# Optimization experiments

Hardware: AMD Instinct MI355X
Metric: run time of the kernel (lower is better)

The kernel has to match this reference:

```python
import jax, jax.numpy as jnp
import numpy as np

B, S, D = 2, 2048, 2048
KVH, QPG, HD = 8, 4, 64          # kv heads, q heads per group, head size
THETA = 1024.0
PARTIAL = 0.5
SOFT_CAP = 50.0
EPS = 1e-5


def setup_inputs() -> dict:
    key = jax.random.key(0)
    ks = jax.random.split(key, 8)
    scale = 0.02
    return {
        "x": jax.random.normal(ks[0], (B, S, D), jnp.float32),
        "wq": jax.random.normal(ks[1], (KVH, QPG, HD, D), jnp.float32) * scale,
        "wk": jax.random.normal(ks[2], (KVH, HD, D), jnp.float32) * scale,
        "wv": jax.random.normal(ks[3], (KVH, HD, D), jnp.float32) * scale,
        "wo": jax.random.normal(ks[4], (D, KVH, QPG, HD), jnp.float32) * scale,
        "qn_w": jnp.ones((HD,), jnp.float32),
        "kn_w": jnp.ones((HD,), jnp.float32),
        "pos_ids": jnp.arange(S, dtype=jnp.int32),
    }


def _rms_norm(t, w):
    var = jnp.mean(jnp.square(t), axis=-1, keepdims=True)
    return t * jax.lax.rsqrt(var + EPS) * w


def _rope_tables(pos_ids):
    half = HD // 2
    rotated_size = int(HD * PARTIAL)
    inv_freq = 1.0 / THETA ** (jnp.arange(0, 2 * half, 2, dtype=jnp.float32) / rotated_size)
    inv_freq = jnp.where(jnp.arange(half) < rotated_size // 2, inv_freq, 0.0)
    freqs = pos_ids.astype(jnp.float32)[:, None] * inv_freq[None, :]   # [S, half]
    emb = jnp.concatenate([freqs, freqs], axis=-1)                      # [S, HD]
    return jnp.cos(emb), jnp.sin(emb)


def _apply_rope(t, cos, sin):
    # t: [..., S, HD]; rotate_half: (x1, x2) -> (-x2, x1)
    half = HD // 2
    x1, x2 = t[..., :half], t[..., half:]
    rot = jnp.concatenate([-x2, x1], axis=-1)
    return t * cos + rot * sin


def reference(x, wq, wk, wv, wo, qn_w, kn_w, pos_ids):
    # QKV projections (GQA)
    q = jnp.einsum("bsd,gphd->bgpsh", x, wq)   # [B,KVH,QPG,S,HD]
    k = jnp.einsum("bsd,ghd->bgsh", x, wk)      # [B,KVH,S,HD]
    v = jnp.einsum("bsd,ghd->bgsh", x, wv)

    # QK-norm (RMS over head dim)
    q = _rms_norm(q, qn_w)
    k = _rms_norm(k, kn_w)

    # partial RoPE
    cos, sin = _rope_tables(pos_ids)            # [S, HD]
    q = _apply_rope(q, cos, sin).astype(x.dtype)
    k = _apply_rope(k, cos, sin).astype(x.dtype)

    # attention in fp32 (upcast_attn) with soft cap and causal mask
    scale = 1.0 / jnp.sqrt(jnp.float32(HD))
    scores = jnp.einsum("bgpsh,bgth->bgpst", q.astype(jnp.float32), k.astype(jnp.float32)) * scale
    scores = SOFT_CAP * jnp.tanh(scores / SOFT_CAP)
    causal = pos_ids[:, None] >= pos_ids[None, :]                    # [S, S]
    scores = jnp.where(causal, scores, jnp.finfo(jnp.float32).min)
    probs = jax.nn.softmax(scores, axis=-1)
    attn = jnp.einsum("bgpst,bgth->bgpsh", probs, v.astype(jnp.float32)).astype(x.dtype)

    # output projection (flatten kv_head x q_heads_per_group -> heads)
    out = jnp.einsum("bgpsh,dgph->bsd", attn, wo)
    return out
```

## Files before the change

### kernel.cpp

```cpp
#include <hip/hip_runtime.h>
#include <stdint.h>

#define S_LEN   2048
#define D_MODEL 2048
#define N_KVH   8
#define N_QPG   4
#define N_HD    64

typedef __attribute__((ext_vector_type(8))) short  short8;
typedef __attribute__((ext_vector_type(4))) short  short4v;
typedef __attribute__((ext_vector_type(4))) float  float4v;

__device__ __forceinline__ unsigned short f2bf(float x) {
    unsigned int u = __float_as_uint(x);
    u = (u + 0x7fffu + ((u >> 16) & 1u)) >> 16;
    return (unsigned short)u;
}

__device__ __forceinline__ void gload_lds16(const unsigned short* g, unsigned short* l) {
    __builtin_amdgcn_global_load_lds((const __attribute__((address_space(1))) unsigned int*)g,
                                     (__attribute__((address_space(3))) unsigned int*)l,
                                     16, 0, 0);
}

__device__ __forceinline__ short8 lds_read8(const unsigned short* p) {
    union { short8 s8; short4v s4[2]; } u;
    u.s4[0] = *(const short4v*)p;
    u.s4[1] = *(const short4v*)(p + 4);
    return u.s8;
}

__global__ __launch_bounds__(256) void cvt_all(const float* __restrict__ x,
                                               const float* __restrict__ wq,
                                               const float* __restrict__ wk,
                                               const float* __restrict__ wv,
                                               const float* __restrict__ wo,
                                               unsigned short* __restrict__ xb,
                                               unsigned short* __restrict__ wqb,
                                               unsigned short* __restrict__ wkb,
                                               unsigned short* __restrict__ wvb,
                                               unsigned short* __restrict__ wob) {
    size_t i = (size_t)blockIdx.x * 256 + threadIdx.x;
    const float* src; unsigned short* dst; size_t off;
    if      (i < 1048576) { src = x;  dst = xb;  off = i; }
    else if (i < 1572864) { src = wq; dst = wqb; off = i - 1048576; }
    else if (i < 1703936) { src = wk; dst = wkb; off = i - 1572864; }
    else if (i < 1835008) { src = wv; dst = wvb; off = i - 1703936; }
    else                  { src = wo; dst = wob; off = i - 1835008; }
    const float4* p = (const float4*)src + off * 2;
    float4 a = p[0], b = p[1];
    union { unsigned short us[8]; uint4 v; } u;
    u.us[0] = f2bf(a.x); u.us[1] = f2bf(a.y); u.us[2] = f2bf(a.z); u.us[3] = f2bf(a.w);
    u.us[4] = f2bf(b.x); u.us[5] = f2bf(b.y); u.us[6] = f2bf(b.z); u.us[7] = f2bf(b.w);
    ((uint4*)dst)[off] = u.v;
}

#define GSTAGE(AL, BL, KO)                         \
    gload_lds16(Ag + (KO),          (AL));         \
    gload_lds16(Ag + 16 * K + (KO), (AL) + 512);   \
    gload_lds16(Bg + (KO),          (BL));         \
    gload_lds16(Bg + 16 * K + (KO), (BL) + 512);

#define GCOMPUTE(OFF)                                                          \
    {                                                                          \
        short8 af[4], bf[4];                                                   \
        _Pragma("unroll")                                                      \
        for (int mt = 0; mt < 4; mt++)                                         \
            af[mt] = *(const short8*)(Alds + (OFF) + (wm + mt * 16 + l15) * 32 + quad * 8); \
        _Pragma("unroll")                                                      \
        for (int nt = 0; nt < 4; nt++)                                         \
            bf[nt] = *(const short8*)(Blds + (OFF) + (wn + nt * 16 + l15) * 32 + quad * 8); \
        _Pragma("unroll")                                                      \
        for (int mt = 0; mt < 4; mt++)                                         \
            _Pragma("unroll")                                                  \
            for (int nt = 0; nt < 4; nt++)                                     \
                acc[mt][nt] = __builtin_amdgcn_mfma_f32_16x16x32_bf16(         \
                    af[mt], bf[nt], acc[mt][nt], 0, 0, 0);                     \
    }

__global__ __launch_bounds__(256)
void gemm_qkv(const unsigned short* __restrict__ xb,
              const unsigned short* __restrict__ wqb,
              const unsigned short* __restrict__ wkb,
              const unsigned short* __restrict__ wvb,
              unsigned short* __restrict__ qout,
              unsigned short* __restrict__ kout,
              unsigned short* __restrict__ vtout,
              const float* __restrict__ qnw,
              const float* __restrict__ knw)
{
    __shared__ __align__(16) unsigned short Alds[2 * 128 * 32];
    __shared__ __align__(16) unsigned short Blds[2 * 128 * 32];

    const int tid  = threadIdx.x;
    const int lane = tid & 63;
    const int wave = tid >> 6;
    const int quad = lane >> 4;
    const int l15  = lane & 15;
    const int bx = blockIdx.x, by = blockIdx.y;
    const int role = (by < 16) ? 0 : (by < 20 ? 1 : 2);
    const unsigned short* A;
    const unsigned short* B;
    int m0, n0;
    if (role == 0)      { A = xb;  B = wqb; m0 = bx * 128; n0 = by * 128; }
    else if (role == 1) { A = xb;  B = wkb; m0 = bx * 128; n0 = (by - 16) * 128; }
    else                { A = wvb; B = xb;  m0 = (by - 20) * 128; n0 = bx * 128; }
    const int K = 2048;
    const int wm = (wave >> 1) * 64;
    const int wn = (wave & 1) * 64;

    float4v acc[4][4];
#pragma unroll
    for (int i = 0; i < 4; i++)
#pragma unroll
        for (int j = 0; j < 4; j++) acc[i][j] = (float4v){0.f, 0.f, 0.f, 0.f};

    const int j0 = wave * 2;
    const int lr = lane >> 2;
    const int lc = (lane & 3) * 8;
    const unsigned short* Ag = A + (size_t)(m0 + j0 * 16 + lr) * K + lc;
    const unsigned short* Bg = B + (size_t)(n0 + j0 * 16 + lr) * K + lc;
    unsigned short* Al0 = Alds + j0 * 512;
    unsigned short* Bl0 = Blds + j0 * 512;
    unsigned short* Al1 = Alds + 4096 + j0 * 512;
    unsigned short* Bl1 = Blds + 4096 + j0 * 512;

    GSTAGE(Al0, Bl0, 0);
    __syncthreads();

    for (int k0 = 0; k0 < K; k0 += 64) {
        GSTAGE(Al1, Bl1, k0 + 32);
        GCOMPUTE(0);
        __syncthreads();
        if (k0 + 64 < K) { GSTAGE(Al0, Bl0, k0 + 64); }
        GCOMPUTE(4096);
        __syncthreads();
    }

    const int nb = n0 + wn;
    const float* nw = (role == 1) ? knw : qnw;
#pragma unroll
    for (int mt = 0; mt < 4; mt++) {
#pragma unroll
        for (int r = 0; r < 4; r++) {
            const int m = m0 + wm + mt * 16 + quad * 4 + r;
            if (role == 2) {
#pragma unroll
                for (int nt = 0; nt < 4; nt++) {
                    int n = nb + nt * 16 + l15;
                    vtout[((size_t)(n >> 11) * 512 + m) * 2048 + (n & 2047)] =
                        f2bf(acc[mt][nt][r]);
                }
            } else {
                float v0 = acc[mt][0][r], v1 = acc[mt][1][r], v2 = acc[mt][2][r], v3 = acc[mt][3][r];
                float s2 = v0 * v0 + v1 * v1 + v2 * v2 + v3 * v3;
#pragma unroll
                for (int off = 1; off < 16; off <<= 1) s2 += __shfl_xor(s2, off, 64);
                float rs = rsqrtf(s2 * (1.0f / 64.0f) + 1e-5f);
                float nv0 = v0 * rs * nw[0 * 16 + l15];
                float nv1 = v1 * rs * nw[1 * 16 + l15];
                float nv2 = v2 * rs * nw[2 * 16 + l15];
                float nv3 = v3 * rs * nw[3 * 16 + l15];
                const int bidx = m >> 11, s = m & 2047;
                float ang = (float)s * exp2f(-0.625f * (float)l15);
                float sn, cs;
                __sincosf(ang, &sn, &cs);
                float o0 = nv0 * cs - nv2 * sn;
                float o2 = nv2 * cs + nv0 * sn;
                unsigned short* dst;
                if (role == 0) {
                    const int g = nb >> 8, p = (nb >> 6) & 3;
                    dst = qout + ((((size_t)bidx * N_KVH + g) * N_QPG + p) * S_LEN + s) * N_HD;
                } else {
                    const int g = nb >> 6;
                    dst = kout + (((size_t)bidx * N_KVH + g) * S_LEN + s) * N_HD;
                }
                dst[0 * 16 + l15] = f2bf(o0);
                dst[1 * 16 + l15] = f2bf(nv1);
                dst[2 * 16 + l15] = f2bf(o2);
                dst[3 * 16 + l15] = f2bf(nv3);
            }
        }
    }
}

__global__ __launch_bounds__(256)
void gemm_out(const unsigned short* __restrict__ A,
              const unsigned short* __restrict__ B,
              float* __restrict__ C,
              int M, int N, int K)
{
    __shared__ __align__(16) unsigned short Alds[2 * 128 * 32];
    __shared__ __align__(16) unsigned short Blds[2 * 128 * 32];

    const int tid  = threadIdx.x;
    const int lane = tid & 63;
    const int wave = tid >> 6;
    const int quad = lane >> 4;
    const int l15  = lane & 15;
    const int m0 = blockIdx.x * 128;
    const int n0 = blockIdx.y * 128;
    const int wm = (wave >> 1) * 64;
    const int wn = (wave & 1) * 64;

    float4v acc[4][4];
#pragma unroll
    for (int i = 0; i < 4; i++)
#pragma unroll
        for (int j = 0; j < 4; j++) acc[i][j] = (float4v){0.f, 0.f, 0.f, 0.f};

    const int j0 = wave * 2;
    const int lr = lane >> 2;
    const int lc = (lane & 3) * 8;
    const unsigned short* Ag = A + (size_t)(m0 + j0 * 16 + lr) * K + lc;
    const unsigned short* Bg = B + (size_t)(n0 + j0 * 16 + lr) * K + lc;
    unsigned short* Al0 = Alds + j0 * 512;
    unsigned short* Bl0 = Blds + j0 * 512;
    unsigned short* Al1 = Alds + 4096 + j0 * 512;
    unsigned short* Bl1 = Blds + 4096 + j0 * 512;

    GSTAGE(Al0, Bl0, 0);
    __syncthreads();

    for (int k0 = 0; k0 < K; k0 += 64) {
        GSTAGE(Al1, Bl1, k0 + 32);
        GCOMPUTE(0);
        __syncthreads();
        if (k0 + 64 < K) { GSTAGE(Al0, Bl0, k0 + 64); }
        GCOMPUTE(4096);
        __syncthreads();
    }

    const int nb = n0 + wn;
#pragma unroll
    for (int mt = 0; mt < 4; mt++) {
#pragma unroll
        for (int r = 0; r < 4; r++) {
            const int m = m0 + wm + mt * 16 + quad * 4 + r;
#pragma unroll
            for (int nt = 0; nt < 4; nt++) {
                int n = nb + nt * 16 + l15;
                C[(size_t)m * N + n] = acc[mt][nt][r];
            }
        }
    }
}

#define PSTRIDE 68

__global__ __launch_bounds__(256)
void attn_kernel(const unsigned short* __restrict__ Q,
                 const unsigned short* __restrict__ Kb,
                 const unsigned short* __restrict__ Vt,
                 unsigned short* __restrict__ O)
{
    __shared__ __align__(16) unsigned short Plds[4 * 32 * PSTRIDE];

    const int tid  = threadIdx.x;
    const int lane = tid & 63;
    const int w    = tid >> 6;
    const int quad = lane >> 4;
    const int l15  = lane & 15;
    const int qx = blockIdx.y;
    const int bg = blockIdx.x;
    const int b = bg >> 3, g = bg & 7;

    const unsigned short* qbase  = Q  + (((size_t)b * N_KVH + g) * N_QPG + w) * S_LEN * N_HD;
    const unsigned short* kbase  = Kb + ((size_t)b * N_KVH + g) * S_LEN * N_HD;
    const unsigned short* vtbase = Vt + ((size_t)b * N_KVH + g) * (size_t)N_HD * S_LEN;

    unsigned short* Pw = Plds + w * (32 * PSTRIDE);

    for (int half = 0; half < 2; half++) {
        const int qt = half ? (63 - qx) : qx;
        const int qrow0 = qt * 32;

        short8 qf[2][2];
#pragma unroll
        for (int mt = 0; mt < 2; mt++)
#pragma unroll
            for (int ks = 0; ks < 2; ks++)
                qf[mt][ks] = *(const short8*)(qbase + (size_t)(qrow0 + mt * 16 + l15) * N_HD + ks * 32 + quad * 8);

        float4v o_acc[2][4];
#pragma unroll
        for (int mt = 0; mt < 2; mt++)
#pragma unroll
            for (int nt = 0; nt < 4; nt++) o_acc[mt][nt] = (float4v){0.f, 0.f, 0.f, 0.f};
        float rsum[2][4];
#pragma unroll
        for (int mt = 0; mt < 2; mt++)
#pragma unroll
            for (int r = 0; r < 4; r++) rsum[mt][r] = 0.f;

        const int ktend = qrow0 >> 6;

        short8 kf[4][2];
#pragma unroll
        for (int nt = 0; nt < 4; nt++)
#pragma unroll
            for (int ks = 0; ks < 2; ks++)
                kf[nt][ks] = *(const short8*)(kbase + (size_t)(nt * 16 + l15) * N_HD + ks * 32 + quad * 8);

        for (int kt = 0; kt <= ktend; kt++) {
            float4v s_acc[2][4];
#pragma unroll
            for (int mt = 0; mt < 2; mt++)
#pragma unroll
                for (int nt = 0; nt < 4; nt++) s_acc[mt][nt] = (float4v){0.f, 0.f, 0.f, 0.f};
            __builtin_amdgcn_s_setprio(1);
#pragma unroll
            for (int ks = 0; ks < 2; ks++)
#pragma unroll
                for (int mt = 0; mt < 2; mt++)
#pragma unroll
                    for (int nt = 0; nt < 4; nt++)
                        s_acc[mt][nt] = __builtin_amdgcn_mfma_f32_16x16x32_bf16(qf[mt][ks], kf[nt][ks], s_acc[mt][nt], 0, 0, 0);
            __builtin_amdgcn_s_setprio(0);

            short8 vf[4][2];
#pragma unroll
            for (int nt = 0; nt < 4; nt++)
#pragma unroll
                for (int ks = 0; ks < 2; ks++)
                    vf[nt][ks] = *(const short8*)(vtbase + (size_t)(nt * 16 + l15) * S_LEN + kt * 64 + ks * 32 + quad * 8);

            if (kt < ktend) {
#pragma unroll
                for (int nt = 0; nt < 4; nt++)
#pragma unroll
                    for (int ks = 0; ks < 2; ks++)
                        kf[nt][ks] = *(const short8*)(kbase + (size_t)((kt + 1) * 64 + nt * 16 + l15) * N_HD + ks * 32 + quad * 8);
            }

            const bool diag = (kt == ktend);
#pragma unroll
            for (int mt = 0; mt < 2; mt++) {
#pragma unroll
                for (int r = 0; r < 4; r++) {
                    const int s_q  = qrow0 + mt * 16 + quad * 4 + r;
                    const int prow = (mt * 16 + quad * 4 + r) * PSTRIDE;
#pragma unroll
                    for (int nt = 0; nt < 4; nt++) {
                        float a = s_acc[mt][nt][r];
                        float u = a * a;
                        float wv = fmaf(u, -3.757018e-7f, 0.18033688f);
                        float p = __builtin_amdgcn_exp2f(fmaf(a, wv, -72.13475204f));
                        if (diag) {
                            int s_k = kt * 64 + nt * 16 + l15;
                            p = (s_k <= s_q) ? p : 0.0f;
                        }
                        rsum[mt][r] += p;
                        Pw[prow + nt * 16 + l15] =
                            (unsigned short)((__float_as_uint(p) + 0x8000u) >> 16);
                    }
                }
            }

#pragma unroll
            for (int ks = 0; ks < 2; ks++) {
                short8 pf[2];
#pragma unroll
                for (int mt = 0; mt < 2; mt++)
                    pf[mt] = lds_read8(Pw + (mt * 16 + l15) * PSTRIDE + ks * 32 + quad * 8);
                __builtin_amdgcn_s_setprio(1);
#pragma unroll
                for (int mt = 0; mt < 2; mt++)
#pragma unroll
                    for (int nt = 0; nt < 4; nt++)
                        o_acc[mt][nt] = __builtin_amdgcn_mfma_f32_16x16x32_bf16(pf[mt], vf[nt][ks], o_acc[mt][nt], 0, 0, 0);
                __builtin_amdgcn_s_setprio(0);
            }
        }

#pragma unroll
        for (int mt = 0; mt < 2; mt++) {
#pragma unroll
            for (int r = 0; r < 4; r++) {
                float s = rsum[mt][r];
                s += __shfl_xor(s, 1, 64);
                s += __shfl_xor(s, 2, 64);
                s += __shfl_xor(s, 4, 64);
                s += __shfl_xor(s, 8, 64);
                float inv = 1.0f / s;
                int s_q = qrow0 + mt * 16 + quad * 4 + r;
                size_t rowoff = ((size_t)(b * S_LEN + s_q)) * D_MODEL + (g * N_QPG + w) * N_HD;
#pragma unroll
                for (int nt = 0; nt < 4; nt++)
                    O[rowoff + nt * 16 + l15] = f2bf(o_acc[mt][nt][r] * inv);
            }
        }
    }
}

extern "C" void kernel_launch(void* const* d_in, const int* in_sizes, int n_in,
                              void* d_out, int out_size, void* d_ws, size_t ws_size,
                              hipStream_t stream)
{
    const float* x    = (const float*)d_in[0];
    const float* wq   = (const float*)d_in[1];
    const float* wk   = (const float*)d_in[2];
    const float* wv   = (const float*)d_in[3];
    const float* wo   = (const float*)d_in[4];
    const float* qn_w = (const float*)d_in[5];
    const float* kn_w = (const float*)d_in[6];

    char* ws = (char*)d_ws;
    unsigned short* xb  = (unsigned short*)(ws + 0);
    unsigned short* wqb = (unsigned short*)(ws + 16777216);
    unsigned short* wkb = (unsigned short*)(ws + 25165824);
    unsigned short* wvb = (unsigned short*)(ws + 27262976);
    unsigned short* wob = (unsigned short*)(ws + 29360128);
    unsigned short* qb  = (unsigned short*)(ws + 37748736);
    unsigned short* kb  = (unsigned short*)(ws + 54525952);
    unsigned short* vt  = (unsigned short*)(ws + 58720256);
    unsigned short* ab  = (unsigned short*)(ws + 62914560);

    cvt_all<<<dim3(9216), 256, 0, stream>>>(x, wq, wk, wv, wo, xb, wqb, wkb, wvb, wob);

    gemm_qkv<<<dim3(32, 24), 256, 0, stream>>>(xb, wqb, wkb, wvb, qb, kb, vt, qn_w, kn_w);

    attn_kernel<<<dim3(16, 32), 256, 0, stream>>>(qb, kb, vt, ab);

    gemm_out<<<dim3(32, 16), 256, 0, stream>>>(ab, wob, (float*)d_out, 4096, 2048, 2048);
}
```

Measured before the change: 382.0 us.

## Software-pipeline attention loop: compute next QK^T scores during current softmax/PV

Restructures the causal attention inner loop so the QK^T MFMAs for tile kt+1 run before the exp/softmax and PV step of tile kt. It uses double-buffered score accumulators and K fragments, with K loaded two tiles ahead, and unrolls the loop by two through a macro. The aim is to overlap the MFMA latency with the VALU exp work and LDS traffic. In exchange it roughly doubles score and K register usage, which could lower occupancy or cause spills.

```diff
diff --git a/kernel.cpp b/kernel.cpp
--- a/kernel.cpp
+++ b/kernel.cpp
@@ -295,83 +295,125 @@
 
         const int ktend = qrow0 >> 6;
 
-        short8 kf[4][2];
+        short8 kfA[4][2], kfB[4][2];
 #pragma unroll
         for (int nt = 0; nt < 4; nt++)
 #pragma unroll
             for (int ks = 0; ks < 2; ks++)
-                kf[nt][ks] = *(const short8*)(kbase + (size_t)(nt * 16 + l15) * N_HD + ks * 32 + quad * 8);
-
-        for (int kt = 0; kt <= ktend; kt++) {
-            float4v s_acc[2][4];
+                kfA[nt][ks] = *(const short8*)(kbase + (size_t)(nt * 16 + l15) * N_HD + ks * 32 + quad * 8);
+
+        float4v sA[2][4], sB[2][4];
+#pragma unroll
+        for (int mt = 0; mt < 2; mt++)
+#pragma unroll
+            for (int nt = 0; nt < 4; nt++) {
+                sA[mt][nt] = (float4v){0.f, 0.f, 0.f, 0.f};
+                sB[mt][nt] = (float4v){0.f, 0.f, 0.f, 0.f};
+            }
+        __builtin_amdgcn_s_setprio(1);
+#pragma unroll
+        for (int ks = 0; ks < 2; ks++)
 #pragma unroll
             for (int mt = 0; mt < 2; mt++)
 #pragma unroll
-                for (int nt = 0; nt < 4; nt++) s_acc[mt][nt] = (float4v){0.f, 0.f, 0.f, 0.f};
-            __builtin_amdgcn_s_setprio(1);
-#pragma unroll
-            for (int ks = 0; ks < 2; ks++)
-#pragma unroll
-                for (int mt = 0; mt < 2; mt++)
-#pragma unroll
-                    for (int nt = 0; nt < 4; nt++)
-                        s_acc[mt][nt] = __builtin_amdgcn_mfma_f32_16x16x32_bf16(qf[mt][ks], kf[nt][ks], s_acc[mt][nt], 0, 0, 0);
-            __builtin_amdgcn_s_setprio(0);
-
-            short8 vf[4][2];
+                for (int nt = 0; nt < 4; nt++)
+                    sA[mt][nt] = __builtin_amdgcn_mfma_f32_16x16x32_bf16(qf[mt][ks], kfA[nt][ks], sA[mt][nt], 0, 0, 0);
+        __builtin_amdgcn_s_setprio(0);
+
+        if (ktend >= 1) {
 #pragma unroll
             for (int nt = 0; nt < 4; nt++)
 #pragma unroll
                 for (int ks = 0; ks < 2; ks++)
-                    vf[nt][ks] = *(const short8*)(vtbase + (size_t)(nt * 16 + l15) * S_LEN + kt * 64 + ks * 32 + quad * 8);
-
-            if (kt < ktend) {
-#pragma unroll
-                for (int nt = 0; nt < 4; nt++)
-#pragma unroll
-                    for (int ks = 0; ks < 2; ks++)
-                        kf[nt][ks] = *(const short8*)(kbase + (size_t)((kt + 1) * 64 + nt * 16 + l15) * N_HD + ks * 32 + quad * 8);
-            }
-
-            const bool diag = (kt == ktend);
-#pragma unroll
-            for (int mt = 0; mt < 2; mt++) {
-#pragma unroll
-                for (int r = 0; r < 4; r++) {
-                    const int s_q  = qrow0 + mt * 16 + quad * 4 + r;
-                    const int prow = (mt * 16 + quad * 4 + r) * PSTRIDE;
-#pragma unroll
-                    for (int nt = 0; nt < 4; nt++) {
-                        float a = s_acc[mt][nt][r];
-                        float u = a * a;
-                        float wv = fmaf(u, -3.757018e-7f, 0.18033688f);
-                        float p = __builtin_amdgcn_exp2f(fmaf(a, wv, -72.13475204f));
-                        if (diag) {
-                            int s_k = kt * 64 + nt * 16 + l15;
-                            p = (s_k <= s_q) ? p : 0.0f;
-                        }
-                        rsum[mt][r] += p;
-                        Pw[prow + nt * 16 + l15] =
-                            (unsigned short)((__float_as_uint(p) + 0x8000u) >> 16);
-                    }
-                }
-            }
-
-#pragma unroll
-            for (int ks = 0; ks < 2; ks++) {
-                short8 pf[2];
-#pragma unroll
-                for (int mt = 0; mt < 2; mt++)
-                    pf[mt] = lds_read8(Pw + (mt * 16 + l15) * PSTRIDE + ks * 32 + quad * 8);
-                __builtin_amdgcn_s_setprio(1);
-#pragma unroll
-                for (int mt = 0; mt < 2; mt++)
-#pragma unroll
-                    for (int nt = 0; nt < 4; nt++)
-                        o_acc[mt][nt] = __builtin_amdgcn_mfma_f32_16x16x32_bf16(pf[mt], vf[nt][ks], o_acc[mt][nt], 0, 0, 0);
-                __builtin_amdgcn_s_setprio(0);
-            }
-        }
+                    kfB[nt][ks] = *(const short8*)(kbase + (size_t)(64 + nt * 16 + l15) * N_HD + ks * 32 + quad * 8);
+        }
+
+#define ASTEP(KT, SC, SN, KFN, KFO)                                            \
+        {                                                                      \
+            const int kt_ = (KT);                                              \
+            short8 vf[4][2];                                                   \
+            _Pragma("unroll")                                                  \
+            for (int nt = 0; nt < 4; nt++)                                     \
+                _Pragma("unroll")                                              \
+                for (int ks = 0; ks < 2; ks++)                                 \
+                    vf[nt][ks] = *(const short8*)(vtbase +                     \
+                        (size_t)(nt * 16 + l15) * S_LEN + kt_ * 64 +           \
+                        ks * 32 + quad * 8);                                   \
+            if (kt_ < ktend) {                                                 \
+                _Pragma("unroll")                                              \
+                for (int mt = 0; mt < 2; mt++)                                 \
+                    _Pragma("unroll")                                          \
+                    for (int nt = 0; nt < 4; nt++)                             \
+                        SN[mt][nt] = (float4v){0.f, 0.f, 0.f, 0.f};            \
+                __builtin_amdgcn_s_setprio(1);                                 \
+                _Pragma("unroll")                                              \
+                for (int ks = 0; ks < 2; ks++)                                 \
+                    _Pragma("unroll")                                          \
+                    for (int mt = 0; mt < 2; mt++)                             \
+                        _Pragma("unroll")                                      \
+                        for (int nt = 0; nt < 4; nt++)                         \
+                            SN[mt][nt] = __builtin_amdgcn_mfma_f32_16x16x32_bf16(\
+                                qf[mt][ks], KFN[nt][ks], SN[mt][nt], 0, 0, 0); \
+                __builtin_amdgcn_s_setprio(0);                                 \
+            }                                                                  \
+            if (kt_ + 2 <= ktend) {                                            \
+                _Pragma("unroll")                                              \
+                for (int nt = 0; nt < 4; nt++)                                 \
+                    _Pragma("unroll")                                          \
+                    for (int ks = 0; ks < 2; ks++)                             \
+                        KFO[nt][ks] = *(const short8*)(kbase +                 \
+                            (size_t)((kt_ + 2) * 64 + nt * 16 + l15) * N_HD +  \
+                            ks * 32 + quad * 8);                               \
+            }                                                                  \
+            const bool diag = (kt_ == ktend);                                  \
+            _Pragma("unroll")                                                  \
+            for (int mt = 0; mt < 2; mt++) {                                   \
+                _Pragma("unroll")                                              \
+                for (int r = 0; r < 4; r++) {                                  \
+                    const int s_q  = qrow0 + mt * 16 + quad * 4 + r;           \
+                    const int prow = (mt * 16 + quad * 4 + r) * PSTRIDE;       \
+                    _Pragma("unroll")                                          \
+                    for (int nt = 0; nt < 4; nt++) {                           \
+                        float a = SC[mt][nt][r];                               \
+                        float u = a * a;                                       \
+                        float wv = fmaf(u, -3.757018e-7f, 0.18033688f);        \
+                        float p = __builtin_amdgcn_exp2f(fmaf(a, wv, -72.13475204f)); \
+                        if (diag) {                                            \
+                            int s_k = kt_ * 64 + nt * 16 + l15;                \
+                            p = (s_k <= s_q) ? p : 0.0f;                       \
+                        }                                                      \
+                        rsum[mt][r] += p;                                      \
+                        Pw[prow + nt * 16 + l15] =                             \
+                            (unsigned short)((__float_as_uint(p) + 0x8000u) >> 16); \
+                    }                                                          \
+                }                                                              \
+            }                                                                  \
+            _Pragma("unroll")                                                  \
+            for (int ks = 0; ks < 2; ks++) {                                   \
+                short8 pf[2];                                                  \
+                _Pragma("unroll")                                              \
+                for (int mt = 0; mt < 2; mt++)                                 \
+                    pf[mt] = lds_read8(Pw + (mt * 16 + l15) * PSTRIDE + ks * 32 + quad * 8); \
+                __builtin_amdgcn_s_setprio(1);                                 \
+                _Pragma("unroll")                                              \
+                for (int mt = 0; mt < 2; mt++)                                 \
+                    _Pragma("unroll")                                          \
+                    for (int nt = 0; nt < 4; nt++)                             \
+                        o_acc[mt][nt] = __builtin_amdgcn_mfma_f32_16x16x32_bf16(\
+                            pf[mt], vf[nt][ks], o_acc[mt][nt], 0, 0, 0);       \
+                __builtin_amdgcn_s_setprio(0);                                 \
+            }                                                                  \
+        }
+
+        int kt = 0;
+        while (kt + 1 <= ktend) {
+            ASTEP(kt,     sA, sB, kfB, kfA);
+            ASTEP(kt + 1, sB, sA, kfA, kfB);
+            kt += 2;
+        }
+        if (kt <= ktend)
+            ASTEP(kt, sA, sB, kfB, kfA);
+#undef ASTEP
 
 #pragma unroll
         for (int mt = 0; mt < 2; mt++) {
```

Result: no change. 387.4 us (+1.4%).

## Switch attention to 32x32x16 MFMA with transposed scores and register-resident P

Applied to the files above, without the earlier changes.

Rewrites the attention inner loop to use 32x32x16 bf16 MFMA with K as the A operand, so each lane holds one query row's scores. The probability tile is packed to bf16 in registers and exchanged across wave halves with shuffles, removing the LDS round-trip for P. The KV tile shrinks from 64 to 32 keys, giving finer causal trimming but more loop iterations. Row sums need only one cross-lane shuffle and output stores become 8-byte packed writes.

```diff
diff --git a/kernel.cpp b/kernel.cpp
--- a/kernel.cpp
+++ b/kernel.cpp
@@ -7,9 +7,10 @@
 #define N_QPG   4
 #define N_HD    64
 
-typedef __attribute__((ext_vector_type(8))) short  short8;
-typedef __attribute__((ext_vector_type(4))) short  short4v;
-typedef __attribute__((ext_vector_type(4))) float  float4v;
+typedef __attribute__((ext_vector_type(8)))  short short8;
+typedef __attribute__((ext_vector_type(4)))  short short4v;
+typedef __attribute__((ext_vector_type(4)))  float float4v;
+typedef __attribute__((ext_vector_type(16))) float floatx16;
 
 __device__ __forceinline__ unsigned short f2bf(float x) {
     unsigned int u = __float_as_uint(x);
@@ -21,13 +22,6 @@
     __builtin_amdgcn_global_load_lds((const __attribute__((address_space(1))) unsigned int*)g,
                                      (__attribute__((address_space(3))) unsigned int*)l,
                                      16, 0, 0);
-}
-
-__device__ __forceinline__ short8 lds_read8(const unsigned short* p) {
-    union { short8 s8; short4v s4[2]; } u;
-    u.s4[0] = *(const short4v*)p;
-    u.s4[1] = *(const short4v*)(p + 4);
-    return u.s8;
 }
 
 __global__ __launch_bounds__(256) void cvt_all(const float* __restrict__ x,
@@ -246,21 +240,20 @@
     }
 }
 
-#define PSTRIDE 68
-
 __global__ __launch_bounds__(256)
 void attn_kernel(const unsigned short* __restrict__ Q,
                  const unsigned short* __restrict__ Kb,
                  const unsigned short* __restrict__ Vt,
                  unsigned short* __restrict__ O)
 {
-    __shared__ __align__(16) unsigned short Plds[4 * 32 * PSTRIDE];
-
     const int tid  = threadIdx.x;
     const int lane = tid & 63;
     const int w    = tid >> 6;
-    const int quad = lane >> 4;
-    const int l15  = lane & 15;
+    const int l31  = lane & 31;
+    const int hi   = lane >> 5;
+    const int hi8  = hi * 8;
+    const int hi4  = hi * 4;
+    const bool lo  = (hi == 0);
     const int qx = blockIdx.y;
     const int bg = blockIdx.x;
     const int b = bg >> 3, g = bg & 7;
@@ -269,125 +262,112 @@
     const unsigned short* kbase  = Kb + ((size_t)b * N_KVH + g) * S_LEN * N_HD;
     const unsigned short* vtbase = Vt + ((size_t)b * N_KVH + g) * (size_t)N_HD * S_LEN;
 
-    unsigned short* Pw = Plds + w * (32 * PSTRIDE);
-
     for (int half = 0; half < 2; half++) {
         const int qt = half ? (63 - qx) : qx;
         const int qrow0 = qt * 32;
-
-        short8 qf[2][2];
-#pragma unroll
-        for (int mt = 0; mt < 2; mt++)
-#pragma unroll
-            for (int ks = 0; ks < 2; ks++)
-                qf[mt][ks] = *(const short8*)(qbase + (size_t)(qrow0 + mt * 16 + l15) * N_HD + ks * 32 + quad * 8);
-
-        float4v o_acc[2][4];
-#pragma unroll
-        for (int mt = 0; mt < 2; mt++)
-#pragma unroll
-            for (int nt = 0; nt < 4; nt++) o_acc[mt][nt] = (float4v){0.f, 0.f, 0.f, 0.f};
-        float rsum[2][4];
-#pragma unroll
-        for (int mt = 0; mt < 2; mt++)
-#pragma unroll
-            for (int r = 0; r < 4; r++) rsum[mt][r] = 0.f;
-
-        const int ktend = qrow0 >> 6;
-
-        short8 kf[4][2];
-#pragma unroll
-        for (int nt = 0; nt < 4; nt++)
-#pragma unroll
-            for (int ks = 0; ks < 2; ks++)
-                kf[nt][ks] = *(const short8*)(kbase + (size_t)(nt * 16 + l15) * N_HD + ks * 32 + quad * 8);
+        const int ktend = qt;
+
+        short8 qf[4];
+#pragma unroll
+        for (int c = 0; c < 4; c++)
+            qf[c] = *(const short8*)(qbase + (size_t)(qrow0 + l31) * N_HD + c * 16 + hi8);
+
+        floatx16 o_acc[2];
+#pragma unroll
+        for (int dt = 0; dt < 2; dt++)
+#pragma unroll
+            for (int i = 0; i < 16; i++) o_acc[dt][i] = 0.f;
+        float rsum = 0.f;
+
+        short8 kf[4];
+#pragma unroll
+        for (int c = 0; c < 4; c++)
+            kf[c] = *(const short8*)(kbase + (size_t)(l31) * N_HD + c * 16 + hi8);
 
         for (int kt = 0; kt <= ktend; kt++) {
-            float4v s_acc[2][4];
-#pragma unroll
-            for (int mt = 0; mt < 2; mt++)
-#pragma unroll
-                for (int nt = 0; nt < 4; nt++) s_acc[mt][nt] = (float4v){0.f, 0.f, 0.f, 0.f};
+            floatx16 s;
+#pragma unroll
+            for (int i = 0; i < 16; i++) s[i] = 0.f;
             __builtin_amdgcn_s_setprio(1);
 #pragma unroll
-            for (int ks = 0; ks < 2; ks++)
-#pragma unroll
-                for (int mt = 0; mt < 2; mt++)
-#pragma unroll
-                    for (int nt = 0; nt < 4; nt++)
-                        s_acc[mt][nt] = __builtin_amdgcn_mfma_f32_16x16x32_bf16(qf[mt][ks], kf[nt][ks], s_acc[mt][nt], 0, 0, 0);
+            for (int c = 0; c < 4; c++)
+                s = __builtin_amdgcn_mfma_f32_32x32x16_bf16(kf[c], qf[c], s, 0, 0, 0);
             __builtin_amdgcn_s_setprio(0);
 
-            short8 vf[4][2];
-#pragma unroll
-            for (int nt = 0; nt < 4; nt++)
-#pragma unroll
-                for (int ks = 0; ks < 2; ks++)
-                    vf[nt][ks] = *(const short8*)(vtbase + (size_t)(nt * 16 + l15) * S_LEN + kt * 64 + ks * 32 + quad * 8);
+            short8 vf00 = *(const short8*)(vtbase + (size_t)(l31)      * S_LEN + kt * 32 + hi8);
+            short8 vf01 = *(const short8*)(vtbase + (size_t)(l31)      * S_LEN + kt * 32 + 16 + hi8);
+            short8 vf10 = *(const short8*)(vtbase + (size_t)(32 + l31) * S_LEN + kt * 32 + hi8);
+            short8 vf11 = *(const short8*)(vtbase + (size_t)(32 + l31) * S_LEN + kt * 32 + 16 + hi8);
 
             if (kt < ktend) {
 #pragma unroll
-                for (int nt = 0; nt < 4; nt++)
-#pragma unroll
-                    for (int ks = 0; ks < 2; ks++)
-                        kf[nt][ks] = *(const short8*)(kbase + (size_t)((kt + 1) * 64 + nt * 16 + l15) * N_HD + ks * 32 + quad * 8);
+                for (int c = 0; c < 4; c++)
+                    kf[c] = *(const short8*)(kbase + (size_t)((kt + 1) * 32 + l31) * N_HD + c * 16 + hi8);
             }
 
             const bool diag = (kt == ktend);
-#pragma unroll
-            for (int mt = 0; mt < 2; mt++) {
-#pragma unroll
-                for (int r = 0; r < 4; r++) {
-                    const int s_q  = qrow0 + mt * 16 + quad * 4 + r;
-                    const int prow = (mt * 16 + quad * 4 + r) * PSTRIDE;
-#pragma unroll
-                    for (int nt = 0; nt < 4; nt++) {
-                        float a = s_acc[mt][nt][r];
-                        float u = a * a;
-                        float wv = fmaf(u, -3.757018e-7f, 0.18033688f);
-                        float p = __builtin_amdgcn_exp2f(fmaf(a, wv, -72.13475204f));
-                        if (diag) {
-                            int s_k = kt * 64 + nt * 16 + l15;
-                            p = (s_k <= s_q) ? p : 0.0f;
-                        }
-                        rsum[mt][r] += p;
-                        Pw[prow + nt * 16 + l15] =
-                            (unsigned short)((__float_as_uint(p) + 0x8000u) >> 16);
-                    }
+            float p[16];
+#pragma unroll
+            for (int r = 0; r < 16; r++) {
+                float a = s[r];
+                float u = a * a;
+                float wv = fmaf(u, -3.757018e-7f, 0.18033688f);
+                float pv = __builtin_amdgcn_exp2f(fmaf(a, wv, -72.13475204f));
+                if (diag) {
+                    int kl = (r & 3) + 8 * (r >> 2) + hi4;
+                    pv = (kl <= l31) ? pv : 0.0f;
                 }
+                rsum += pv;
+                p[r] = pv;
             }
 
-#pragma unroll
-            for (int ks = 0; ks < 2; ks++) {
-                short8 pf[2];
-#pragma unroll
-                for (int mt = 0; mt < 2; mt++)
-                    pf[mt] = lds_read8(Pw + (mt * 16 + l15) * PSTRIDE + ks * 32 + quad * 8);
-                __builtin_amdgcn_s_setprio(1);
-#pragma unroll
-                for (int mt = 0; mt < 2; mt++)
-#pragma unroll
-                    for (int nt = 0; nt < 4; nt++)
-                        o_acc[mt][nt] = __builtin_amdgcn_mfma_f32_16x16x32_bf16(pf[mt], vf[nt][ks], o_acc[mt][nt], 0, 0, 0);
-                __builtin_amdgcn_s_setprio(0);
-            }
+            unsigned X0, X1, Y0, Y1, Z0, Z1, W0, W1;
+            asm("v_cvt_pk_bf16_f32 %0, %1, %2" : "=v"(X0) : "v"(p[0]),  "v"(p[1]));
+            asm("v_cvt_pk_bf16_f32 %0, %1, %2" : "=v"(X1) : "v"(p[2]),  "v"(p[3]));
+            asm("v_cvt_pk_bf16_f32 %0, %1, %2" : "=v"(Y0) : "v"(p[4]),  "v"(p[5]));
+            asm("v_cvt_pk_bf16_f32 %0, %1, %2" : "=v"(Y1) : "v"(p[6]),  "v"(p[7]));
+            asm("v_cvt_pk_bf16_f32 %0, %1, %2" : "=v"(Z0) : "v"(p[8]),  "v"(p[9]));
+            asm("v_cvt_pk_bf16_f32 %0, %1, %2" : "=v"(Z1) : "v"(p[10]), "v"(p[11]));
+            asm("v_cvt_pk_bf16_f32 %0, %1, %2" : "=v"(W0) : "v"(p[12]), "v"(p[13]));
+            asm("v_cvt_pk_bf16_f32 %0, %1, %2" : "=v"(W1) : "v"(p[14]), "v"(p[15]));
+            unsigned sX0 = (unsigned)__shfl_xor((int)X0, 32, 64);
+            unsigned sX1 = (unsigned)__shfl_xor((int)X1, 32, 64);
+            unsigned sY0 = (unsigned)__shfl_xor((int)Y0, 32, 64);
+            unsigned sY1 = (unsigned)__shfl_xor((int)Y1, 32, 64);
+            unsigned sZ0 = (unsigned)__shfl_xor((int)Z0, 32, 64);
+            unsigned sZ1 = (unsigned)__shfl_xor((int)Z1, 32, 64);
+            unsigned sW0 = (unsigned)__shfl_xor((int)W0, 32, 64);
+            unsigned sW1 = (unsigned)__shfl_xor((int)W1, 32, 64);
+            union { unsigned u[4]; short8 s8; } pb0, pb1;
+            pb0.u[0] = lo ? X0  : sY0;
+            pb0.u[1] = lo ? X1  : sY1;
+            pb0.u[2] = lo ? sX0 : Y0;
+            pb0.u[3] = lo ? sX1 : Y1;
+            pb1.u[0] = lo ? Z0  : sW0;
+            pb1.u[1] = lo ? Z1  : sW1;
+            pb1.u[2] = lo ? sZ0 : W0;
+            pb1.u[3] = lo ? sZ1 : W1;
+
+            __builtin_amdgcn_s_setprio(1);
+            o_acc[0] = __builtin_amdgcn_mfma_f32_32x32x16_bf16(vf00, pb0.s8, o_acc[0], 0, 0, 0);
+            o_acc[0] = __builtin_amdgcn_mfma_f32_32x32x16_bf16(vf01, pb1.s8, o_acc[0], 0, 0, 0);
+            o_acc[1] = __builtin_amdgcn_mfma_f32_32x32x16_bf16(vf10, pb0.s8, o_acc[1], 0, 0, 0);
+            o_acc[1] = __builtin_amdgcn_mfma_f32_32x32x16_bf16(vf11, pb1.s8, o_acc[1], 0, 0, 0);
+            __builtin_amdgcn_s_setprio(0);
         }
 
-#pragma unroll
-        for (int mt = 0; mt < 2; mt++) {
-#pragma unroll
-            for (int r = 0; r < 4; r++) {
-                float s = rsum[mt][r];
-                s += __shfl_xor(s, 1, 64);
-                s += __shfl_xor(s, 2, 64);
-                s += __shfl_xor(s, 4, 64);
-                s += __shfl_xor(s, 8, 64);
-                float inv = 1.0f / s;
-                int s_q = qrow0 + mt * 16 + quad * 4 + r;
-                size_t rowoff = ((size_t)(b * S_LEN + s_q)) * D_MODEL + (g * N_QPG + w) * N_HD;
-#pragma unroll
-                for (int nt = 0; nt < 4; nt++)
-                    O[rowoff + nt * 16 + l15] = f2bf(o_acc[mt][nt][r] * inv);
+        rsum += __shfl_xor(rsum, 32, 64);
+        float inv = 1.0f / rsum;
+        size_t rowoff = ((size_t)(b * S_LEN + qrow0 + l31)) * D_MODEL + (g * N_QPG + w) * N_HD;
+#pragma unroll
+        for (int dt = 0; dt < 2; dt++) {
+#pragma unroll
+            for (int gg = 0; gg < 4; gg++) {
+                union { unsigned short us[4]; unsigned long long v; } pk;
+#pragma unroll
+                for (int j = 0; j < 4; j++)
+                    pk.us[j] = f2bf(o_acc[dt][gg * 4 + j] * inv);
+                *(unsigned long long*)(O + rowoff + dt * 32 + gg * 8 + hi4) = pk.v;
             }
         }
     }
```

After: 380.0 us. Within noise of the previous version (-0.5%).
